# Kernel optimization log

Hardware: AMD Instinct MI355X
Metric: run time of the kernel (lower is better)

Reference implementation:

```python
import jax, jax.numpy as jnp
import numpy as np

B = 128      # graphs
N = 32       # atoms per graph (fixed)
NODES = B * N
E = B * N * N  # fully-connected edges incl. self-loops
H = 256      # hidden_dim
TD = 128     # time_dim
TYPE = 100   # type_dim
NF = 10      # frac_emb_freq
EDGE_DIM = NF * 2 * 3 + 6  # 66
L = 4        # num_layers
EPS = 1e-5


def _edges():
    idx = jnp.arange(NODES).reshape(B, N)
    ei = jnp.broadcast_to(idx[:, :, None], (B, N, N)).reshape(-1)  # row (target)
    ej = jnp.broadcast_to(idx[:, None, :], (B, N, N)).reshape(-1)  # col (source)
    return ei, ej


def _layernorm(x, g, b):
    mu = jnp.mean(x, axis=-1, keepdims=True)
    var = jnp.mean((x - mu) ** 2, axis=-1, keepdims=True)
    return (x - mu) * jax.lax.rsqrt(var + EPS) * g + b


def setup_inputs() -> dict:
    key = jax.random.key(0)
    ks = jax.random.split(key, 32)
    p = lambda k, shp: (jax.random.normal(k, shp, dtype=jnp.float32) * 0.02)
    inp = {
        "t": jax.random.uniform(ks[0], (B,), dtype=jnp.float32),
        "atom_types": jax.random.normal(ks[1], (NODES, TYPE), dtype=jnp.float32),
        "frac_coords": jax.random.uniform(ks[2], (NODES, 3), dtype=jnp.float32),
        "l_polar": jax.random.normal(ks[3], (B, 6), dtype=jnp.float32),
        "node2graph": jnp.repeat(jnp.arange(B, dtype=jnp.int32), N),
        # type_smooth
        "Ws": p(ks[4], (TYPE, H)), "bs": jnp.zeros((H,), jnp.float32),
        # node_embedding
        "Wn": p(ks[5], (H + TD, H)), "bn": jnp.zeros((H,), jnp.float32),
        # per-layer params, stacked over L
        "ln_g": jnp.ones((L, H), jnp.float32), "ln_b": jnp.zeros((L, H), jnp.float32),
        "m1_W": p(ks[6], (L, 2 * H + EDGE_DIM, H)), "m1_b": jnp.zeros((L, H), jnp.float32),
        "m2_W": p(ks[7], (L, H, H)), "m2_b": jnp.zeros((L, H), jnp.float32),
        "a1_W": p(ks[8], (L, 2 * H, H)), "a1_b": jnp.zeros((L, H), jnp.float32),
        "a2_W": p(ks[9], (L, H, H)), "a2_b": jnp.zeros((L, H), jnp.float32),
        # final layer norm + readouts
        "fln_g": jnp.ones((H,), jnp.float32), "fln_b": jnp.zeros((H,), jnp.float32),
        "type_W": p(ks[10], (H, TYPE)), "type_b": jnp.zeros((TYPE,), jnp.float32),
        "polar_W": p(ks[11], (H, 6)),
        "frac_W": p(ks[12], (H, 3)),
    }
    return inp


def reference(t, atom_types, frac_coords, l_polar, node2graph,
              Ws, bs, Wn, bn, ln_g, ln_b, m1_W, m1_b, m2_W, m2_b,
              a1_W, a1_b, a2_W, a2_b, fln_g, fln_b, type_W, type_b,
              polar_W, frac_W):
    ei, ej = _edges()
    edge2graph = node2graph[ei]

    # ---- node features: type_smooth + sinusoidal time embedding ----
    half = TD // 2
    tfreq = jnp.exp(jnp.arange(half, dtype=jnp.float32) * (-np.log(10000.0) / (half - 1)))
    targ = t[:, None] * tfreq[None, :]                       # [B, half]
    time_emb = jnp.concatenate([jnp.sin(targ), jnp.cos(targ)], axis=-1)  # [B, TD]
    time_emb = jnp.repeat(time_emb, N, axis=0)               # [NODES, TD]
    type_emb = atom_types @ Ws + bs                           # [NODES, H]
    nf = jnp.concatenate([type_emb, time_emb], axis=-1) @ Wn + bn  # [NODES, H]

    # ---- edge features: sinusoidal frac-diff embedding + l_polar ----
    d = jnp.mod(frac_coords[ej] - frac_coords[ei], 1.0)       # [E, 3]
    ffreq = 2.0 * np.pi * jnp.arange(NF, dtype=jnp.float32)
    femb = (d[:, :, None] * ffreq[None, None, :]).reshape(E, NF * 3)
    femb = jnp.concatenate([jnp.sin(femb), jnp.cos(femb)], axis=-1)  # [E, 60]
    ef = jnp.concatenate([femb, l_polar[edge2graph]], axis=-1)       # [E, 66]

    # ---- GNN layers ----
    ones = jnp.ones((E,), jnp.float32)
    cnt = jax.ops.segment_sum(ones, ei, num_segments=NODES)          # [NODES]
    cnt = jnp.maximum(cnt, 1.0)[:, None]
    for i in range(L):
        h = _layernorm(nf, ln_g[i], ln_b[i])
        mij = jnp.concatenate([h[ei], h[ej], ef], axis=-1)           # [E, 2H+66]
        mij = jax.nn.silu(mij @ m1_W[i] + m1_b[i])
        mij = jax.nn.silu(mij @ m2_W[i] + m2_b[i])                   # [E, H]
        msg = jax.ops.segment_sum(mij, ei, num_segments=NODES) / cnt  # scatter-mean
        a = jnp.concatenate([nf, msg], axis=-1)
        a = jax.nn.silu(a @ a1_W[i] + a1_b[i])
        a = jax.nn.silu(a @ a2_W[i] + a2_b[i])
        nf = nf + a

    nf = _layernorm(nf, fln_g, fln_b)
    gsum = jax.ops.segment_sum(nf, node2graph, num_segments=B)
    gcnt = jnp.maximum(jax.ops.segment_sum(jnp.ones((NODES,), jnp.float32), node2graph, num_segments=B), 1.0)
    graph_features = gsum / gcnt[:, None]

    type_pred = nf @ type_W + type_b
    l_polar_pred = graph_features @ polar_W
    frac_coords_pred = nf @ frac_W
    return type_pred, l_polar_pred, frac_coords_pred
```

## Files before the change

### kernel.cpp

```cpp
#include <hip/hip_runtime.h>
#include <hip/hip_bf16.h>

typedef __attribute__((ext_vector_type(8))) short short8;
typedef __attribute__((ext_vector_type(4))) short short4v;
typedef __attribute__((ext_vector_type(4))) float float4v;
typedef __bf16 bf16x8 __attribute__((ext_vector_type(8)));

#define MFMA16(A,B,C) __builtin_amdgcn_mfma_f32_16x16x32_bf16( \
    __builtin_bit_cast(bf16x8,(A)), __builtin_bit_cast(bf16x8,(B)), (C), 0, 0, 0)

static __device__ __forceinline__ float bf2f(unsigned short b){
  unsigned u = ((unsigned)b) << 16; float f; __builtin_memcpy(&f,&u,sizeof(f)); return f;
}
static __device__ __forceinline__ unsigned short f2bf(float f){
  __bf16 h = (__bf16)f;
  return __builtin_bit_cast(unsigned short, h);
}
static __device__ __forceinline__ float siluf(float x){
  return x * __builtin_amdgcn_rcpf(1.0f + __expf(-x));
}
static __device__ __forceinline__ float ldf(const float* p, size_t i){ return p[i]; }
static __device__ __forceinline__ float ldf(const unsigned short* p, size_t i){ return bf2f(p[i]); }

static __device__ __forceinline__ void gemm_body(
    const unsigned short* __restrict__ A, int lda,
    const unsigned short* __restrict__ Bp, int KT, int NT,
    const float* __restrict__ bias,
    float* __restrict__ outF, int ldoF,
    unsigned short* __restrict__ outH, int ldoH,
    const float* __restrict__ res,
    int Nc, int flags, int bx, int by)
{
  const int w = threadIdx.x >> 6, lane = threadIdx.x & 63;
  const int l15 = lane & 15, q = lane >> 4;
  const int rowL = bx * 64 + w * 16;
  const int colB = by * 64;
  const short8* pa = (const short8*)(A + (size_t)(rowL + l15) * lda);
  const short8* pb = (const short8*)Bp;
  float4v acc[4] = {};
  int ntc[4];
  #pragma unroll
  for (int i = 0; i < 4; ++i){ int t = (colB >> 4) + i; ntc[i] = t < NT ? t : NT - 1; }
  for (int kt = 0; kt < KT; ++kt){
    short8 a = pa[kt * 4 + q];
    #pragma unroll
    for (int i = 0; i < 4; ++i){
      short8 b = pb[(size_t)(kt * NT + ntc[i]) * 64 + lane];
      acc[i] = MFMA16(a, b, acc[i]);
    }
  }
  const bool doB = flags & 2, doS = flags & 1, doR = flags & 4;
  #pragma unroll
  for (int i = 0; i < 4; ++i){
    int c = colB + i * 16 + l15;
    if (c >= Nc) continue;
    float bv = doB ? bias[c] : 0.0f;
    #pragma unroll
    for (int r = 0; r < 4; ++r){
      int row = rowL + q * 4 + r;
      float v = acc[i][r] + bv;
      if (doS) v = siluf(v);
      if (doR) v += res[(size_t)row * ldoF + c];
      if (outF) outF[(size_t)row * ldoF + c] = v;
      if (outH) outH[(size_t)row * ldoH + c] = f2bf(v);
    }
  }
}

__global__ __launch_bounds__(256) void k_gemm(
    const unsigned short* __restrict__ A, int lda,
    const unsigned short* __restrict__ Bp, int KT, int NT,
    const float* __restrict__ bias,
    float* __restrict__ outF, int ldoF,
    unsigned short* __restrict__ outH, int ldoH,
    const float* __restrict__ res,
    int Nc, int flags)
{
  gemm_body(A, lda, Bp, KT, NT, bias, outF, ldoF, outH, ldoH, res, Nc, flags,
            blockIdx.x, blockIdx.y);
}

__global__ __launch_bounds__(256) void k_out(
    const unsigned short* __restrict__ h, const unsigned short* __restrict__ gf,
    const unsigned short* __restrict__ typep, const float* __restrict__ typeb,
    const unsigned short* __restrict__ polarp, const unsigned short* __restrict__ fracp,
    float* __restrict__ out)
{
  int b = blockIdx.x;
  if (b < 128){
    gemm_body(h, 256, typep, 8, 7, typeb, out, 100,
              (unsigned short*)nullptr, 0, (const float*)nullptr, 100, 2,
              b & 63, b >> 6);
  } else if (b < 130){
    gemm_body(gf, 256, polarp, 8, 1, (const float*)nullptr, out + 409600, 6,
              (unsigned short*)nullptr, 0, (const float*)nullptr, 6, 0,
              b - 128, 0);
  } else {
    gemm_body(h, 256, fracp, 8, 1, (const float*)nullptr, out + 410368, 3,
              (unsigned short*)nullptr, 0, (const float*)nullptr, 3, 0,
              b - 130, 0);
  }
}

template<typename T>
static __device__ __forceinline__ void pack_tile(
    const T* W, int ldw, int Krows, int Ncols,
    unsigned short* dst, int NTtot, int ntoff, int kt, int nt,
    const float* addrow, int lane)
{
  int l15 = lane & 15, q = lane >> 4;
  int col = nt * 16 + l15;
  int kr0 = kt * 32 + q * 8;
  short8 v;
  #pragma unroll
  for (int j = 0; j < 8; ++j){
    int r = kr0 + j;
    float x = 0.0f;
    if (r < Krows && col < Ncols){
      x = ldf(W, (size_t)r * ldw + col);
      if (addrow) x += addrow[(r >> 5) * 256 + col];
    }
    v[j] = (short)f2bf(x);
  }
  ((short8*)dst)[(size_t)(kt * NTtot + ntoff + nt) * 64 + lane] = v;
}

static __device__ __forceinline__ void packW_dispatch(
    int b, int lane,
    const float* Ws, const float* Wn,
    const float* typeW, const float* polarW, const float* fracW,
    const float* m1W, const float* m2W, const float* a1W, const float* a2W,
    unsigned short* Wsp, unsigned short* Wnp, unsigned short* typep,
    unsigned short* polarp, unsigned short* fracp,
    unsigned short* W12p, unsigned short* W1botp, unsigned short* W2Tp,
    unsigned short* a1p, unsigned short* a2p)
{
  if (b < 64)      { pack_tile(Ws,    256, 100, 256, Wsp,   16, 0, b >> 4, b & 15, nullptr, lane); return; }
  if (b < 256){ int s = b - 64;  pack_tile(Wn,    256, 384, 256, Wnp,   16, 0, s >> 4, s & 15, nullptr, lane); return; }
  if (b < 312){ int s = b - 256; pack_tile(typeW, 100, 256, 100, typep,  7, 0, s / 7,  s % 7,  nullptr, lane); return; }
  if (b < 320){ int s = b - 312; pack_tile(polarW,  6, 256,   6, polarp, 1, 0, s, 0, nullptr, lane); return; }
  if (b < 328){ int s = b - 320; pack_tile(fracW,   3, 256,   3, fracp,  1, 0, s, 0, nullptr, lane); return; }
  int s2 = b - 328;
  int l = s2 / 800, bb = s2 % 800;
  const float* m1Wl = m1W + (size_t)l * 578 * 256;
  const float* m2Wl = m2W + (size_t)l * 65536;
  const float* a1Wl = a1W + (size_t)l * 131072;
  const float* a2Wl = a2W + (size_t)l * 65536;
  unsigned short* W12pl   = W12p   + (size_t)l * 131072;
  unsigned short* W1botpl = W1botp + (size_t)l * 16384;
  unsigned short* W2Tpl   = W2Tp   + (size_t)l * 65536;
  unsigned short* a1pl    = a1p    + (size_t)l * 131072;
  unsigned short* a2pl    = a2p    + (size_t)l * 65536;
  if (bb < 128)       pack_tile(m1Wl,           256, 256, 256, W12pl,  32,  0, bb >> 4, bb & 15, nullptr, lane);
  else if (bb < 256){ int s = bb - 128; pack_tile(m1Wl + 256*256, 256, 256, 256, W12pl,  32, 16, s >> 4, s & 15, nullptr, lane); }
  else if (bb < 288){ int s = bb - 256; pack_tile(m1Wl + 512*256, 256,  64, 256, W1botpl,16,  0, s >> 4, s & 15, nullptr, lane); }
  else if (bb < 416){ int s = bb - 288; pack_tile(m2Wl,           256, 256, 256, W2Tpl,  16,  0, s >> 4, s & 15, nullptr, lane); }
  else if (bb < 672){ int s = bb - 416; pack_tile(a1Wl,           256, 512, 256, a1pl,   16,  0, s >> 4, s & 15, nullptr, lane); }
  else              { int s = bb - 672; pack_tile(a2Wl,           256, 256, 256, a2pl,   16,  0, s >> 4, s & 15, nullptr, lane); }
}

__global__ void k_prep(
    const float* Ws, const float* Wn,
    const float* typeW, const float* polarW, const float* fracW,
    const float* m1W, const float* m2W, const float* a1W, const float* a2W,
    unsigned short* Wsp, unsigned short* Wnp, unsigned short* typep,
    unsigned short* polarp, unsigned short* fracp,
    unsigned short* W12p, unsigned short* W1botp, unsigned short* W2Tp,
    unsigned short* a1p, unsigned short* a2p,
    const float* at, const float* t, const float* fc,
    const float* lpol, const float* m1b,
    unsigned short* atp, unsigned short* cat1,
    unsigned short* femb, float* lpw)
{
  int b0 = blockIdx.x;
  if (b0 < 882){
    int tile = b0 * 4 + (threadIdx.x >> 6);
    packW_dispatch(tile, threadIdx.x & 63, Ws, Wn, typeW, polarW, fracW,
                   m1W, m2W, a1W, a2W, Wsp, Wnp, typep, polarp, fracp,
                   W12p, W1botp, W2Tp, a1p, a2p);
    return;
  }
  int b = b0 - 882;
  if (b < 2048){
    int id = b * 256 + threadIdx.x;
    int r = id >> 7, c = id & 127;
    atp[id] = (c < 100) ? f2bf(at[r * 100 + c]) : (unsigned short)0;
  } else if (b < 2176){
    int g = b - 2048, i = threadIdx.x;
    if (i < 128){
      float tg = t[g];
      int f = i & 63;
      float fr = __expf((-9.210340371976184f / 63.0f) * (float)f);
      float arg = tg * fr;
      float v = (i < 64) ? __sinf(arg) : __cosf(arg);
      unsigned short hv = f2bf(v);
      for (int n = 0; n < 32; ++n)
        cat1[(size_t)(g * 32 + n) * 384 + 256 + i] = hv;
    }
  } else if (b < 2688){
    int e = (b - 2176) * 256 + threadIdx.x;
    int g = e >> 10, i = (e >> 5) & 31, j = e & 31;
    int nt = g * 32 + i, ns = g * 32 + j;
    unsigned short o[64];
    #pragma unroll
    for (int k = 0; k < 3; ++k){
      float d = fc[ns * 3 + k] - fc[nt * 3 + k];
      d -= floorf(d);
      #pragma unroll
      for (int f = 0; f < 10; ++f){
        float ang = d * (6.283185307179586f * (float)f);
        o[k * 10 + f]      = f2bf(__sinf(ang));
        o[30 + k * 10 + f] = f2bf(__cosf(ang));
      }
    }
    #pragma unroll
    for (int z = 60; z < 64; ++z) o[z] = 0;
    short8* dst = (short8*)(femb + (size_t)e * 64);
    #pragma unroll
    for (int v = 0; v < 8; ++v){
      short8 s;
      #pragma unroll
      for (int j2 = 0; j2 < 8; ++j2) s[j2] = (short)o[v * 8 + j2];
      dst[v] = s;
    }
  } else {
    int s = b - 2688;
    int l = s >> 7, g = s & 127, c = threadIdx.x;
    const float* W = m1W + (size_t)l * 578 * 256;
    float acc = m1b[l * 256 + c];
    #pragma unroll
    for (int k = 0; k < 6; ++k)
      acc += lpol[g * 6 + k] * W[(572 + k) * 256 + c];
    lpw[((size_t)l * 128 + g) * 256 + c] = acc;
  }
}

#define HLD 264

__global__ __launch_bounds__(256) void k_lnP(
    const float* __restrict__ nf, const float* __restrict__ g_,
    const float* __restrict__ b_,
    const unsigned short* __restrict__ W12p, const float* __restrict__ lpwl,
    unsigned short* __restrict__ P1, unsigned short* __restrict__ P2)
{
  __shared__ unsigned short hld[32 * HLD];
  const int w = threadIdx.x >> 6, lane = threadIdx.x & 63;
  const int l15 = lane & 15, q = lane >> 4;
  const int g = blockIdx.x >> 2, q4 = blockIdx.x & 3;
  #pragma unroll
  for (int rr = 0; rr < 8; ++rr){
    int row = w * 8 + rr;
    float4v x = *(const float4v*)(nf + ((size_t)(g*32+row))*256 + lane*4);
    float s = x[0]+x[1]+x[2]+x[3];
    #pragma unroll
    for (int m=1;m<64;m<<=1) s += __shfl_xor(s,m,64);
    float mu = s * (1.f/256.f);
    float d0=x[0]-mu,d1=x[1]-mu,d2=x[2]-mu,d3=x[3]-mu;
    float vs=d0*d0+d1*d1+d2*d2+d3*d3;
    #pragma unroll
    for (int m=1;m<64;m<<=1) vs += __shfl_xor(vs,m,64);
    float rs = rsqrtf(vs*(1.f/256.f)+1e-5f);
    float4v gg = *(const float4v*)(g_ + lane*4);
    float4v bb = *(const float4v*)(b_ + lane*4);
    short4v o;
    o[0]=(short)f2bf(d0*rs*gg[0]+bb[0]);
    o[1]=(short)f2bf(d1*rs*gg[1]+bb[1]);
    o[2]=(short)f2bf(d2*rs*gg[2]+bb[2]);
    o[3]=(short)f2bf(d3*rs*gg[3]+bb[3]);
    *(short4v*)(&hld[row*HLD + lane*4]) = o;
  }
  __syncthreads();
  float4v acc[2][2] = {};
  const short8* pb = (const short8*)W12p;
  for (int kt = 0; kt < 8; ++kt){
    short8 a0 = *(const short8*)(&hld[(size_t)l15*HLD + kt*32 + q*8]);
    short8 a1 = *(const short8*)(&hld[(size_t)(16+l15)*HLD + kt*32 + q*8]);
    #pragma unroll
    for (int i = 0; i < 2; ++i){
      short8 bfr = pb[(size_t)(kt*32 + q4*8 + w*2 + i)*64 + lane];
      acc[0][i] = MFMA16(a0, bfr, acc[0][i]);
      acc[1][i] = MFMA16(a1, bfr, acc[1][i]);
    }
  }
  unsigned short* dst = (q4 < 2) ? P1 : P2;
  const int cho = (q4 & 1) * 128;
  #pragma unroll
  for (int i = 0; i < 2; ++i){
    int ch = cho + (w*2 + i)*16 + l15;
    float lv = (q4 < 2) ? lpwl[g*256 + ch] : 0.0f;
    #pragma unroll
    for (int mt = 0; mt < 2; ++mt){
      #pragma unroll
      for (int r = 0; r < 4; ++r){
        int node = g*32 + mt*16 + q*4 + r;
        dst[(size_t)node*256 + ch] = f2bf(acc[mt][i][r] + lv);
      }
    }
  }
}

__global__ __launch_bounds__(256) void k_a12(
    const unsigned short* __restrict__ cat2,
    const unsigned short* __restrict__ a1pl, const float* __restrict__ a1bl,
    const unsigned short* __restrict__ a2pl, const float* __restrict__ a2bl,
    float* __restrict__ nf, unsigned short* __restrict__ cat2w)
{
  __shared__ unsigned short t1[16 * HLD];
  const int w = threadIdx.x >> 6, lane = threadIdx.x & 63;
  const int l15 = lane & 15, q = lane >> 4;
  const int r0 = (blockIdx.x >> 1) * 16, h2 = blockIdx.x & 1;
  const short8* pb1 = (const short8*)a1pl;
  const short8* pb2 = (const short8*)a2pl;
  float4v acc[4] = {};
  for (int kt = 0; kt < 16; ++kt){
    short8 a0 = *(const short8*)(cat2 + (size_t)(r0 + l15)*512 + kt*32 + q*8);
    #pragma unroll
    for (int i = 0; i < 4; ++i){
      short8 bfr = pb1[(size_t)(kt*16 + w*4 + i)*64 + lane];
      acc[i] = MFMA16(a0, bfr, acc[i]);
    }
  }
  #pragma unroll
  for (int i = 0; i < 4; ++i){
    int c = (w*4+i)*16 + l15;
    float bv = a1bl[c];
    #pragma unroll
    for (int r = 0; r < 4; ++r)
      t1[(size_t)(q*4 + r)*HLD + c] = f2bf(siluf(acc[i][r] + bv));
  }
  __syncthreads();
  float4v c2[2] = {};
  for (int kt = 0; kt < 8; ++kt){
    short8 a0 = *(const short8*)(&t1[(size_t)l15*HLD + kt*32 + q*8]);
    #pragma unroll
    for (int i = 0; i < 2; ++i){
      short8 bfr = pb2[(size_t)(kt*16 + h2*8 + w*2 + i)*64 + lane];
      c2[i] = MFMA16(a0, bfr, c2[i]);
    }
  }
  #pragma unroll
  for (int i = 0; i < 2; ++i){
    int c = h2*128 + (w*2+i)*16 + l15;
    float bv = a2bl[c];
    #pragma unroll
    for (int r = 0; r < 4; ++r){
      int row = r0 + q*4 + r;
      float v = nf[(size_t)row*256 + c] + siluf(c2[i][r] + bv);
      nf[(size_t)row*256 + c] = v;
      cat2w[(size_t)row*512 + c] = f2bf(v);
    }
  }
}

__global__ __launch_bounds__(256) void k_lnF(
    const float* __restrict__ nf, const float* __restrict__ g_,
    const float* __restrict__ b_,
    unsigned short* __restrict__ h, unsigned short* __restrict__ gf)
{
  __shared__ unsigned short hld[32 * HLD];
  const int w = threadIdx.x >> 6, lane = threadIdx.x & 63;
  const int g = blockIdx.x;
  #pragma unroll
  for (int rr = 0; rr < 8; ++rr){
    int row = w * 8 + rr;
    float4v x = *(const float4v*)(nf + ((size_t)(g*32+row))*256 + lane*4);
    float s = x[0]+x[1]+x[2]+x[3];
    #pragma unroll
    for (int m=1;m<64;m<<=1) s += __shfl_xor(s,m,64);
    float mu = s * (1.f/256.f);
    float d0=x[0]-mu,d1=x[1]-mu,d2=x[2]-mu,d3=x[3]-mu;
    float vs=d0*d0+d1*d1+d2*d2+d3*d3;
    #pragma unroll
    for (int m=1;m<64;m<<=1) vs += __shfl_xor(vs,m,64);
    float rs = rsqrtf(vs*(1.f/256.f)+1e-5f);
    float4v gg = *(const float4v*)(g_ + lane*4);
    float4v bb = *(const float4v*)(b_ + lane*4);
    short4v o;
    o[0]=(short)f2bf(d0*rs*gg[0]+bb[0]);
    o[1]=(short)f2bf(d1*rs*gg[1]+bb[1]);
    o[2]=(short)f2bf(d2*rs*gg[2]+bb[2]);
    o[3]=(short)f2bf(d3*rs*gg[3]+bb[3]);
    *(short4v*)(&hld[row*HLD + lane*4]) = o;
    *(short4v*)(h + ((size_t)(g*32+row))*256 + lane*4) = o;
  }
  __syncthreads();
  int c = threadIdx.x;
  float s = 0.0f;
  #pragma unroll
  for (int n = 0; n < 32; ++n) s += bf2f(hld[n*HLD + c]);
  gf[g*256 + c] = f2bf(s * (1.0f/32.0f));
}

#define EST 268
__global__ __launch_bounds__(256, 4) void k_edge(
    const unsigned short* __restrict__ femb,
    const unsigned short* __restrict__ W1botp,
    const unsigned short* __restrict__ P1,
    const unsigned short* __restrict__ P2,
    const unsigned short* __restrict__ W2Tp,
    const float* __restrict__ b2,
    unsigned short* __restrict__ cat2)
{
  __shared__ unsigned short M1[64 * EST];
  const int w = threadIdx.x >> 6, lane = threadIdx.x & 63;
  const int l15 = lane & 15, q = lane >> 4;
  const int b = blockIdx.x, g = b >> 4;
  const int n0 = (b & 15) * 2;
  const int cb = w * 64;
  const short8* fb8  = (const short8*)femb;
  const short8* w1b8 = (const short8*)W1botp;
  const short8* w2t8 = (const short8*)W2Tp;

  short4v p1v[2][4], p2v[2][4];
  #pragma unroll
  for (int ct = 0; ct < 4; ++ct){
    int co = cb + ct*16 + q*4;
    p1v[0][ct] = *(const short4v*)(P1 + (size_t)(g*32 + n0    )*256 + co);
    p1v[1][ct] = *(const short4v*)(P1 + (size_t)(g*32 + n0 + 1)*256 + co);
    p2v[0][ct] = *(const short4v*)(P2 + (size_t)(g*32 +      l15)*256 + co);
    p2v[1][ct] = *(const short4v*)(P2 + (size_t)(g*32 + 16 + l15)*256 + co);
  }

  float4v acc[4][4] = {};
  #pragma unroll
  for (int ks = 0; ks < 2; ++ks){
    short8 a[4];
    #pragma unroll
    for (int ct = 0; ct < 4; ++ct)
      a[ct] = w1b8[(size_t)(ks * 16 + w * 4 + ct) * 64 + lane];
    #pragma unroll
    for (int et = 0; et < 4; ++et){
      int edge = b * 64 + et * 16 + l15;
      short8 bf = fb8[(size_t)edge * 8 + ks * 4 + q];
      #pragma unroll
      for (int ct = 0; ct < 4; ++ct)
        acc[ct][et] = MFMA16(a[ct], bf, acc[ct][et]);
    }
  }
  #pragma unroll
  for (int ct = 0; ct < 4; ++ct)
    #pragma unroll
    for (int et = 0; et < 4; ++et){
      short4v sv;
      #pragma unroll
      for (int r = 0; r < 4; ++r){
        float v = acc[ct][et][r] + bf2f(p1v[et>>1][ct][r]) + bf2f(p2v[et&1][ct][r]);
        sv[r] = (short)f2bf(siluf(v));
      }
      *(short4v*)(&M1[(size_t)(et * 16 + l15) * EST + cb + ct * 16 + q * 4]) = sv;
    }
  __syncthreads();
  float4v c2[4][4] = {};
  for (int kt = 0; kt < 8; ++kt){
    short8 a[4];
    #pragma unroll
    for (int ct = 0; ct < 4; ++ct)
      a[ct] = w2t8[(size_t)(kt * 16 + w * 4 + ct) * 64 + lane];
    #pragma unroll
    for (int et = 0; et < 4; ++et){
      short8 m = *(const short8*)(&M1[(size_t)(et * 16 + l15) * EST + kt * 32 + q * 8]);
      #pragma unroll
      for (int ct = 0; ct < 4; ++ct)
        c2[ct][et] = MFMA16(m, a[ct], c2[ct][et]);
    }
  }
  #pragma unroll
  for (int ct = 0; ct < 4; ++ct){
    float bv = b2[cb + ct * 16 + l15];
    #pragma unroll
    for (int nn = 0; nn < 2; ++nn){
      float s = siluf(c2[ct][2*nn  ][0] + bv) + siluf(c2[ct][2*nn  ][1] + bv)
              + siluf(c2[ct][2*nn  ][2] + bv) + siluf(c2[ct][2*nn  ][3] + bv)
              + siluf(c2[ct][2*nn+1][0] + bv) + siluf(c2[ct][2*nn+1][1] + bv)
              + siluf(c2[ct][2*nn+1][2] + bv) + siluf(c2[ct][2*nn+1][3] + bv);
      s += __shfl_xor(s, 16, 64);
      s += __shfl_xor(s, 32, 64);
      if (q == 0)
        cat2[(size_t)(b*2 + nn) * 512 + 256 + cb + ct * 16 + l15] =
            f2bf(s * (1.0f / 32.0f));
    }
  }
}

extern "C" void kernel_launch(void* const* d_in, const int* in_sizes, int n_in,
                              void* d_out, int out_size, void* d_ws, size_t ws_size,
                              hipStream_t stream)
{
  const float* t      = (const float*)d_in[0];
  const float* at     = (const float*)d_in[1];
  const float* fc     = (const float*)d_in[2];
  const float* lpol   = (const float*)d_in[3];
  const float* Ws     = (const float*)d_in[5];
  const float* bs     = (const float*)d_in[6];
  const float* Wn     = (const float*)d_in[7];
  const float* bn     = (const float*)d_in[8];
  const float* ln_g   = (const float*)d_in[9];
  const float* ln_b   = (const float*)d_in[10];
  const float* m1W    = (const float*)d_in[11];
  const float* m1b    = (const float*)d_in[12];
  const float* m2W    = (const float*)d_in[13];
  const float* m2b    = (const float*)d_in[14];
  const float* a1W    = (const float*)d_in[15];
  const float* a1b    = (const float*)d_in[16];
  const float* a2W    = (const float*)d_in[17];
  const float* a2b    = (const float*)d_in[18];
  const float* flng   = (const float*)d_in[19];
  const float* flnb   = (const float*)d_in[20];
  const float* typeW  = (const float*)d_in[21];
  const float* typeb  = (const float*)d_in[22];
  const float* polarW = (const float*)d_in[23];
  const float* fracW  = (const float*)d_in[24];
  float* out = (float*)d_out;

  char* ws = (char*)d_ws;
  size_t off = 0;
  auto alloc = [&](size_t bytes) -> char* {
    char* p = ws + off; off += (bytes + 255) & ~(size_t)255; return p;
  };
  float*          nf    = (float*)         alloc((size_t)4096*256*4);
  unsigned short* cat2  = (unsigned short*)alloc((size_t)4096*512*2);
  unsigned short* h     = (unsigned short*)alloc((size_t)4096*256*2);
  unsigned short* cat1  = (unsigned short*)alloc((size_t)4096*384*2);
  unsigned short* atp   = (unsigned short*)alloc((size_t)4096*128*2);
  unsigned short* femb  = (unsigned short*)alloc((size_t)131072*64*2);
  float*          lpw   = (float*)         alloc((size_t)4*128*256*4);
  unsigned short* P1    = (unsigned short*)alloc((size_t)4096*256*2);
  unsigned short* P2    = (unsigned short*)alloc((size_t)4096*256*2);
  unsigned short* gf    = (unsigned short*)alloc((size_t)128*256*2);
  unsigned short* Wsp   = (unsigned short*)alloc((size_t)4*16*1024);
  unsigned short* Wnp   = (unsigned short*)alloc((size_t)12*16*1024);
  unsigned short* typep = (unsigned short*)alloc((size_t)8*7*1024);
  unsigned short* polarp= (unsigned short*)alloc((size_t)8*1*1024);
  unsigned short* fracp = (unsigned short*)alloc((size_t)8*1*1024);
  unsigned short* W12p  = (unsigned short*)alloc((size_t)4*131072*2);
  unsigned short* W1botp= (unsigned short*)alloc((size_t)4*16384*2);
  unsigned short* W2Tp  = (unsigned short*)alloc((size_t)4*65536*2);
  unsigned short* a1p   = (unsigned short*)alloc((size_t)4*131072*2);
  unsigned short* a2p   = (unsigned short*)alloc((size_t)4*65536*2);

  k_prep<<<dim3(4082), dim3(256), 0, stream>>>(Ws, Wn, typeW, polarW, fracW,
      m1W, m2W, a1W, a2W,
      Wsp, Wnp, typep, polarp, fracp, W12p, W1botp, W2Tp, a1p, a2p,
      at, t, fc, lpol, m1b, atp, cat1, femb, lpw);
  k_gemm<<<dim3(64,4), dim3(256), 0, stream>>>(atp, 128, Wsp, 4, 16, bs,
      (float*)nullptr, 0, cat1, 384, (const float*)nullptr, 256, 2);
  k_gemm<<<dim3(64,4), dim3(256), 0, stream>>>(cat1, 384, Wnp, 12, 16, bn,
      nf, 256, cat2, 512, (const float*)nullptr, 256, 2);

  for (int l = 0; l < 4; ++l){
    k_lnP<<<dim3(512), dim3(256), 0, stream>>>(nf, ln_g + l*256, ln_b + l*256,
        W12p + (size_t)l*131072, lpw + (size_t)l*32768, P1, P2);
    k_edge<<<dim3(2048), dim3(256), 0, stream>>>(femb, W1botp + (size_t)l*16384,
        P1, P2, W2Tp + (size_t)l*65536, m2b + l*256, cat2);
    k_a12<<<dim3(512), dim3(256), 0, stream>>>(cat2, a1p + (size_t)l*131072,
        a1b + l*256, a2p + (size_t)l*65536, a2b + l*256, nf, cat2);
  }

  k_lnF<<<dim3(128), dim3(256), 0, stream>>>(nf, flng, flnb, h, gf);
  k_out<<<dim3(194), dim3(256), 0, stream>>>(h, gf, typep, typeb,
                                             polarp, fracp, out);
}
```

Before: 366.9 us.

## Fuse next-layer LayerNorm and projections into a12, and final LN with readouts

The node-update kernel now also computes the next layer's LayerNorm and the P1/P2 projections for its 16 rows, so the separate per-layer k_lnP launch is removed except for the first layer. The final LayerNorm kernel also performs the type, frac and polar readout GEMMs from shared memory, which drops k_out and the h/gf intermediate buffers. Launch count and global round trips go down, but k_a12P now runs only 256 blocks, each computing all 256 output columns plus a 512-wide projection, so parallelism drops and per-block work rises.

```diff
diff --git a/kernel.cpp b/kernel.cpp
--- a/kernel.cpp
+++ b/kernel.cpp
@@ -78,28 +78,6 @@
 {
   gemm_body(A, lda, Bp, KT, NT, bias, outF, ldoF, outH, ldoH, res, Nc, flags,
             blockIdx.x, blockIdx.y);
-}
-
-__global__ __launch_bounds__(256) void k_out(
-    const unsigned short* __restrict__ h, const unsigned short* __restrict__ gf,
-    const unsigned short* __restrict__ typep, const float* __restrict__ typeb,
-    const unsigned short* __restrict__ polarp, const unsigned short* __restrict__ fracp,
-    float* __restrict__ out)
-{
-  int b = blockIdx.x;
-  if (b < 128){
-    gemm_body(h, 256, typep, 8, 7, typeb, out, 100,
-              (unsigned short*)nullptr, 0, (const float*)nullptr, 100, 2,
-              b & 63, b >> 6);
-  } else if (b < 130){
-    gemm_body(gf, 256, polarp, 8, 1, (const float*)nullptr, out + 409600, 6,
-              (unsigned short*)nullptr, 0, (const float*)nullptr, 6, 0,
-              b - 128, 0);
-  } else {
-    gemm_body(h, 256, fracp, 8, 1, (const float*)nullptr, out + 410368, 3,
-              (unsigned short*)nullptr, 0, (const float*)nullptr, 3, 0,
-              b - 130, 0);
-  }
 }
 
 template<typename T>
@@ -299,16 +277,21 @@
   }
 }
 
-__global__ __launch_bounds__(256) void k_a12(
+__global__ __launch_bounds__(256) void k_a12P(
     const unsigned short* __restrict__ cat2,
     const unsigned short* __restrict__ a1pl, const float* __restrict__ a1bl,
     const unsigned short* __restrict__ a2pl, const float* __restrict__ a2bl,
-    float* __restrict__ nf, unsigned short* __restrict__ cat2w)
-{
-  __shared__ unsigned short t1[16 * HLD];
+    float* __restrict__ nf, unsigned short* __restrict__ cat2w,
+    const float* __restrict__ lng, const float* __restrict__ lnb,
+    const unsigned short* __restrict__ W12p, const float* __restrict__ lpwl,
+    unsigned short* __restrict__ P1, unsigned short* __restrict__ P2, int doP)
+{
+  __shared__ float nf32[16 * 260];
+  __shared__ unsigned short sh[16 * HLD];
   const int w = threadIdx.x >> 6, lane = threadIdx.x & 63;
   const int l15 = lane & 15, q = lane >> 4;
-  const int r0 = (blockIdx.x >> 1) * 16, h2 = blockIdx.x & 1;
+  const int r0 = blockIdx.x * 16;
+  const int g = blockIdx.x >> 1;
   const short8* pb1 = (const short8*)a1pl;
   const short8* pb2 = (const short8*)a2pl;
   float4v acc[4] = {};
@@ -326,21 +309,21 @@
     float bv = a1bl[c];
     #pragma unroll
     for (int r = 0; r < 4; ++r)
-      t1[(size_t)(q*4 + r)*HLD + c] = f2bf(siluf(acc[i][r] + bv));
+      sh[(size_t)(q*4 + r)*HLD + c] = f2bf(siluf(acc[i][r] + bv));
   }
   __syncthreads();
-  float4v c2[2] = {};
+  float4v c2[4] = {};
   for (int kt = 0; kt < 8; ++kt){
-    short8 a0 = *(const short8*)(&t1[(size_t)l15*HLD + kt*32 + q*8]);
-    #pragma unroll
-    for (int i = 0; i < 2; ++i){
-      short8 bfr = pb2[(size_t)(kt*16 + h2*8 + w*2 + i)*64 + lane];
+    short8 a0 = *(const short8*)(&sh[(size_t)l15*HLD + kt*32 + q*8]);
+    #pragma unroll
+    for (int i = 0; i < 4; ++i){
+      short8 bfr = pb2[(size_t)(kt*16 + w*4 + i)*64 + lane];
       c2[i] = MFMA16(a0, bfr, c2[i]);
     }
   }
   #pragma unroll
-  for (int i = 0; i < 2; ++i){
-    int c = h2*128 + (w*2+i)*16 + l15;
+  for (int i = 0; i < 4; ++i){
+    int c = (w*4+i)*16 + l15;
     float bv = a2bl[c];
     #pragma unroll
     for (int r = 0; r < 4; ++r){
@@ -348,17 +331,69 @@
       float v = nf[(size_t)row*256 + c] + siluf(c2[i][r] + bv);
       nf[(size_t)row*256 + c] = v;
       cat2w[(size_t)row*512 + c] = f2bf(v);
-    }
-  }
-}
-
-__global__ __launch_bounds__(256) void k_lnF(
+      nf32[(q*4 + r)*260 + c] = v;
+    }
+  }
+  if (!doP) return;
+  __syncthreads();
+  #pragma unroll
+  for (int rr = 0; rr < 4; ++rr){
+    int row = w * 4 + rr;
+    float4v x = *(const float4v*)(&nf32[row*260 + lane*4]);
+    float s = x[0]+x[1]+x[2]+x[3];
+    #pragma unroll
+    for (int m=1;m<64;m<<=1) s += __shfl_xor(s,m,64);
+    float mu = s * (1.f/256.f);
+    float d0=x[0]-mu,d1=x[1]-mu,d2=x[2]-mu,d3=x[3]-mu;
+    float vs=d0*d0+d1*d1+d2*d2+d3*d3;
+    #pragma unroll
+    for (int m=1;m<64;m<<=1) vs += __shfl_xor(vs,m,64);
+    float rs = rsqrtf(vs*(1.f/256.f)+1e-5f);
+    float4v gg = *(const float4v*)(lng + lane*4);
+    float4v bb = *(const float4v*)(lnb + lane*4);
+    short4v o;
+    o[0]=(short)f2bf(d0*rs*gg[0]+bb[0]);
+    o[1]=(short)f2bf(d1*rs*gg[1]+bb[1]);
+    o[2]=(short)f2bf(d2*rs*gg[2]+bb[2]);
+    o[3]=(short)f2bf(d3*rs*gg[3]+bb[3]);
+    *(short4v*)(&sh[row*HLD + lane*4]) = o;
+  }
+  __syncthreads();
+  float4v pc[8] = {};
+  const short8* pb = (const short8*)W12p;
+  for (int kt = 0; kt < 8; ++kt){
+    short8 a0 = *(const short8*)(&sh[(size_t)l15*HLD + kt*32 + q*8]);
+    #pragma unroll
+    for (int i = 0; i < 8; ++i){
+      short8 bfr = pb[(size_t)(kt*32 + w*8 + i)*64 + lane];
+      pc[i] = MFMA16(a0, bfr, pc[i]);
+    }
+  }
+  #pragma unroll
+  for (int i = 0; i < 8; ++i){
+    int nt = w*8 + i;
+    unsigned short* dst = (nt < 16) ? P1 : P2;
+    int ch = (nt & 15)*16 + l15;
+    float lv = (nt < 16) ? lpwl[g*256 + ch] : 0.0f;
+    #pragma unroll
+    for (int r = 0; r < 4; ++r){
+      int node = r0 + q*4 + r;
+      dst[(size_t)node*256 + ch] = f2bf(pc[i][r] + lv);
+    }
+  }
+}
+
+__global__ __launch_bounds__(256) void k_lnFO(
     const float* __restrict__ nf, const float* __restrict__ g_,
     const float* __restrict__ b_,
-    unsigned short* __restrict__ h, unsigned short* __restrict__ gf)
-{
-  __shared__ unsigned short hld[32 * HLD];
+    const unsigned short* __restrict__ typep, const float* __restrict__ typeb,
+    const unsigned short* __restrict__ polarp,
+    const unsigned short* __restrict__ fracp,
+    float* __restrict__ out)
+{
+  __shared__ unsigned short hld[33 * HLD];
   const int w = threadIdx.x >> 6, lane = threadIdx.x & 63;
+  const int l15 = lane & 15, q = lane >> 4;
   const int g = blockIdx.x;
   #pragma unroll
   for (int rr = 0; rr < 8; ++rr){
@@ -381,14 +416,70 @@
     o[2]=(short)f2bf(d2*rs*gg[2]+bb[2]);
     o[3]=(short)f2bf(d3*rs*gg[3]+bb[3]);
     *(short4v*)(&hld[row*HLD + lane*4]) = o;
-    *(short4v*)(h + ((size_t)(g*32+row))*256 + lane*4) = o;
   }
   __syncthreads();
-  int c = threadIdx.x;
-  float s = 0.0f;
-  #pragma unroll
-  for (int n = 0; n < 32; ++n) s += bf2f(hld[n*HLD + c]);
-  gf[g*256 + c] = f2bf(s * (1.0f/32.0f));
+  {
+    int c = threadIdx.x;
+    float s = 0.0f;
+    #pragma unroll
+    for (int n = 0; n < 32; ++n) s += bf2f(hld[n*HLD + c]);
+    hld[32*HLD + c] = f2bf(s * (1.0f/32.0f));
+  }
+  __syncthreads();
+  {
+    float4v tacc[2][2] = {};
+    const short8* pb = (const short8*)typep;
+    for (int kt = 0; kt < 8; ++kt){
+      short8 a0 = *(const short8*)(&hld[(size_t)l15*HLD + kt*32 + q*8]);
+      short8 a1 = *(const short8*)(&hld[(size_t)(16+l15)*HLD + kt*32 + q*8]);
+      #pragma unroll
+      for (int i = 0; i < 2; ++i){
+        int nt = w + i*4; if (nt > 6) nt = 6;
+        short8 bfr = pb[(size_t)(kt*7 + nt)*64 + lane];
+        tacc[0][i] = MFMA16(a0, bfr, tacc[0][i]);
+        tacc[1][i] = MFMA16(a1, bfr, tacc[1][i]);
+      }
+    }
+    #pragma unroll
+    for (int i = 0; i < 2; ++i){
+      int c = (w + i*4)*16 + l15;
+      if (c < 100){
+        float bv = typeb[c];
+        #pragma unroll
+        for (int mt = 0; mt < 2; ++mt)
+          #pragma unroll
+          for (int r = 0; r < 4; ++r){
+            int node = g*32 + mt*16 + q*4 + r;
+            out[(size_t)node*100 + c] = tacc[mt][i][r] + bv;
+          }
+      }
+    }
+  }
+  if (w < 2){
+    float4v facc = {};
+    const short8* pb = (const short8*)fracp;
+    for (int kt = 0; kt < 8; ++kt){
+      short8 a0 = *(const short8*)(&hld[(size_t)(w*16 + l15)*HLD + kt*32 + q*8]);
+      facc = MFMA16(a0, pb[(size_t)kt*64 + lane], facc);
+    }
+    if (l15 < 3){
+      #pragma unroll
+      for (int r = 0; r < 4; ++r){
+        int node = g*32 + w*16 + q*4 + r;
+        out[410368 + (size_t)node*3 + l15] = facc[r];
+      }
+    }
+  }
+  if (w == 3){
+    float4v pacc = {};
+    const short8* pb = (const short8*)polarp;
+    for (int kt = 0; kt < 8; ++kt){
+      short8 a0 = *(const short8*)(&hld[(size_t)32*HLD + kt*32 + q*8]);
+      pacc = MFMA16(a0, pb[(size_t)kt*64 + lane], pacc);
+    }
+    if (q == 0 && l15 < 6)
+      out[409600 + (size_t)g*6 + l15] = pacc[0];
+  }
 }
 
 #define EST 268
@@ -519,14 +610,12 @@
   };
   float*          nf    = (float*)         alloc((size_t)4096*256*4);
   unsigned short* cat2  = (unsigned short*)alloc((size_t)4096*512*2);
-  unsigned short* h     = (unsigned short*)alloc((size_t)4096*256*2);
   unsigned short* cat1  = (unsigned short*)alloc((size_t)4096*384*2);
   unsigned short* atp   = (unsigned short*)alloc((size_t)4096*128*2);
   unsigned short* femb  = (unsigned short*)alloc((size_t)131072*64*2);
   float*          lpw   = (float*)         alloc((size_t)4*128*256*4);
   unsigned short* P1    = (unsigned short*)alloc((size_t)4096*256*2);
   unsigned short* P2    = (unsigned short*)alloc((size_t)4096*256*2);
-  unsigned short* gf    = (unsigned short*)alloc((size_t)128*256*2);
   unsigned short* Wsp   = (unsigned short*)alloc((size_t)4*16*1024);
   unsigned short* Wnp   = (unsigned short*)alloc((size_t)12*16*1024);
   unsigned short* typep = (unsigned short*)alloc((size_t)8*7*1024);
@@ -546,17 +635,18 @@
       (float*)nullptr, 0, cat1, 384, (const float*)nullptr, 256, 2);
   k_gemm<<<dim3(64,4), dim3(256), 0, stream>>>(cat1, 384, Wnp, 12, 16, bn,
       nf, 256, cat2, 512, (const float*)nullptr, 256, 2);
+  k_lnP<<<dim3(512), dim3(256), 0, stream>>>(nf, ln_g, ln_b, W12p, lpw, P1, P2);
 
   for (int l = 0; l < 4; ++l){
-    k_lnP<<<dim3(512), dim3(256), 0, stream>>>(nf, ln_g + l*256, ln_b + l*256,
-        W12p + (size_t)l*131072, lpw + (size_t)l*32768, P1, P2);
+    int ln = (l + 1 < 4) ? l + 1 : 3;
     k_edge<<<dim3(2048), dim3(256), 0, stream>>>(femb, W1botp + (size_t)l*16384,
         P1, P2, W2Tp + (size_t)l*65536, m2b + l*256, cat2);
-    k_a12<<<dim3(512), dim3(256), 0, stream>>>(cat2, a1p + (size_t)l*131072,
-        a1b + l*256, a2p + (size_t)l*65536, a2b + l*256, nf, cat2);
-  }
-
-  k_lnF<<<dim3(128), dim3(256), 0, stream>>>(nf, flng, flnb, h, gf);
-  k_out<<<dim3(194), dim3(256), 0, stream>>>(h, gf, typep, typeb,
-                                             polarp, fracp, out);
-}
+    k_a12P<<<dim3(256), dim3(256), 0, stream>>>(cat2, a1p + (size_t)l*131072,
+        a1b + l*256, a2p + (size_t)l*65536, a2b + l*256, nf, cat2,
+        ln_g + ln*256, ln_b + ln*256, W12p + (size_t)ln*131072,
+        lpw + (size_t)ln*32768, P1, P2, (l < 3) ? 1 : 0);
+  }
+
+  k_lnFO<<<dim3(128), dim3(256), 0, stream>>>(nf, flng, flnb,
+      typep, typeb, polarp, fracp, out);
+}
```

Result: no change. 364.1 us (-0.8%).
